# Kernel optimization log

Hardware: AMD Instinct MI355X
Metric: run time of the kernel (lower is better)

## Reference

```python
import jax, jax.numpy as jnp
import numpy as np

NSAMPLE = 32
EPS = 1e-5


def _fps(xyz, npoint):
    # xyz: [B, N, 3] -> indices [B, npoint] (farthest point sampling, start at idx 0)
    B, N, _ = xyz.shape
    def body(i, state):
        idx, dist, far = state
        idx = idx.at[:, i].set(far)
        centroid = jnp.take_along_axis(xyz, far[:, None, None], axis=1)  # [B,1,3]
        d = jnp.sum((xyz - centroid) ** 2, axis=-1)                      # [B,N]
        dist = jnp.minimum(dist, d)
        far = jnp.argmax(dist, axis=-1).astype(jnp.int32)
        return idx, dist, far
    idx0 = jnp.zeros((B, npoint), jnp.int32)
    dist0 = jnp.full((B, N), 1e10, xyz.dtype)
    far0 = jnp.zeros((B,), jnp.int32)
    idx, _, _ = jax.lax.fori_loop(0, npoint, body, (idx0, dist0, far0))
    return idx


def _knn(query, ref, k):
    # query [B,S,3], ref [B,N,3] -> neighbor idx [B,S,k]
    d = (jnp.sum(query * query, -1)[:, :, None]
         - 2.0 * jnp.einsum('bsc,bnc->bsn', query, ref)
         + jnp.sum(ref * ref, -1)[:, None, :])
    _, idx = jax.lax.top_k(-d, k)
    return idx


def _gather(x, idx):
    # x [B,N,C], idx [B,S,K] -> [B,S,K,C]
    B, S, K = idx.shape
    out = jnp.take_along_axis(x, idx.reshape(B, S * K)[..., None], axis=1)
    return out.reshape(B, S, K, x.shape[-1])


def _set_abstraction(xyz, feat, npoint, weights):
    # xyz [B,N,3], feat [B,N,C]
    fidx = _fps(xyz, npoint)
    new_xyz = jnp.take_along_axis(xyz, fidx[..., None], axis=1)        # [B,S,3]
    nidx = _knn(new_xyz, xyz, NSAMPLE)                                 # [B,S,K]
    g_xyz = _gather(xyz, nidx) - new_xyz[:, :, None, :]                # [B,S,K,3]
    g_feat = _gather(feat, nidx)                                       # [B,S,K,C]
    x = jnp.concatenate([g_xyz, g_feat], axis=-1)                      # [B,S,K,3+C]
    for W in weights:  # 1x1 conv == per-point matmul, then InstanceNorm2d (affine=False) + ReLU
        x = jnp.einsum('bskc,cd->bskd', x, W)
        mu = jnp.mean(x, axis=(1, 2), keepdims=True)
        var = jnp.var(x, axis=(1, 2), keepdims=True)
        x = jax.nn.relu((x - mu) * jax.lax.rsqrt(var + EPS))
    new_feat = jnp.max(x, axis=2)                                      # [B,S,Cout]
    return new_xyz, new_feat, fidx


def setup_inputs() -> dict:
    key = jax.random.key(0)
    ks = jax.random.split(key, 8)
    B, N = 4, 16384
    pc = jax.random.normal(ks[0], (B, 3, N), jnp.float32)
    feature = jax.random.normal(ks[1], (B, 3, N), jnp.float32)
    def w(k, cin, cout):
        return jax.random.normal(k, (cin, cout), jnp.float32) / np.sqrt(cin).astype(np.float32)
    return {
        'pc': pc, 'feature': feature,
        'sa1_w1': w(ks[2], 6, 32),  'sa1_w2': w(ks[3], 32, 32), 'sa1_w3': w(ks[4], 32, 32),
        'sa2_w1': w(ks[5], 35, 64), 'sa2_w2': w(ks[6], 64, 64), 'sa2_w3': w(ks[7], 64, 64),
    }


def reference(pc, feature, sa1_w1, sa1_w2, sa1_w3, sa2_w1, sa2_w2, sa2_w3):
    NPOINT = 4096
    xyz = jnp.transpose(pc, (0, 2, 1))       # [B,N,3]
    feat = jnp.transpose(feature, (0, 2, 1))  # [B,N,3]
    xyz1, feat1, fidx1 = _set_abstraction(xyz, feat, NPOINT // 2, [sa1_w1, sa1_w2, sa1_w3])
    xyz2, feat2, fidx2 = _set_abstraction(xyz1, feat1, NPOINT // 4, [sa2_w1, sa2_w2, sa2_w3])
    # match torch channel-first layout on outputs
    pc_l1 = jnp.transpose(xyz1, (0, 2, 1))
    pc_l2 = jnp.transpose(xyz2, (0, 2, 1))
    feat_l2 = jnp.transpose(feat2, (0, 2, 1))  # [B,64,NPOINT//4]
    return (pc, pc_l1, pc_l2, feat_l2, fidx1, fidx2)
```

## Files before the change

kernel.cpp:

```cpp
#include <hip/hip_runtime.h>
#include <math.h>

namespace {

constexpr int BB = 4;
constexpr int N0 = 16384;
constexpr int S1 = 2048;
constexpr int S2 = 1024;

__device__ __forceinline__ float sq3(float x, float y, float z){
  #pragma clang fp contract(off)
  return x*x + y*y + z*z;
}
__device__ __forceinline__ float sqdist(float ax,float ay,float az,float bx,float by,float bz){
  #pragma clang fp contract(off)
  float dx = ax-bx; float dy = ay-by; float dz = az-bz;
  return dx*dx + dy*dy + dz*dz;
}
__device__ __forceinline__ float dot3(float ax,float ay,float az,float bx,float by,float bz){
  #pragma clang fp contract(off)
  return ax*bx + ay*by + az*bz;
}
__device__ __forceinline__ float knndist(float qs, float dot, float rs){
  #pragma clang fp contract(off)
  return (qs - 2.0f*dot) + rs;
}

__global__ __launch_bounds__(256) void k_setup(const float* __restrict__ pc,
                                               const float* __restrict__ feat,
                                               float* __restrict__ out_pc,
                                               float* __restrict__ xyz,
                                               float* __restrict__ fN,
                                               float* __restrict__ rsq0)
{
  int t = blockIdx.x*256 + threadIdx.x;
  if (t < BB*3*N0) out_pc[t] = pc[t];
  if (t < BB*N0){
    int b = t >> 14, n = t & (N0-1);
    const float* p = pc + (size_t)b*3*N0;
    float x = p[n], y = p[N0+n], z = p[2*N0+n];
    float* q = xyz + (size_t)t*3;
    q[0]=x; q[1]=y; q[2]=z;
    rsq0[t] = sq3(x,y,z);
    const float* f = feat + (size_t)b*3*N0;
    float* g = fN + (size_t)t*3;
    g[0]=f[n]; g[1]=f[N0+n]; g[2]=f[2*N0+n];
  }
}

__device__ __forceinline__ void fps_writeout(int b, int i, float cx, float cy, float cz, int far,
                                             float* sxyz, float* srsq, float* pcl, float* fidxf, int NP)
{
  fidxf[(size_t)b*NP + i] = (float)far;
  float* o = sxyz + ((size_t)b*NP + i)*3;
  o[0]=cx; o[1]=cy; o[2]=cz;
  float* pb = pcl + (size_t)b*3*NP;
  pb[i] = cx; pb[NP+i] = cy; pb[2*NP+i] = cz;
  srsq[(size_t)b*NP + i] = sq3(cx,cy,cz);
}

template<int N, int NP, int BS, int PPT>
__global__ __launch_bounds__(BS, 2) void k_fps(const float* __restrict__ pts,
                                               float* __restrict__ sxyz,
                                               float* __restrict__ srsq,
                                               float* __restrict__ pcl,
                                               float* __restrict__ fidxf)
{
  static_assert(N == BS*PPT, "bad fps shape");
  constexpr int NW = BS/64;
  int b = blockIdx.x, t = threadIdx.x;
  int lane = t & 63;
  int wid  = t >> 6;
  const float* P = pts + (size_t)b*N*3;

  __shared__ unsigned long long slot[2][NW];

  float px[PPT], py[PPT], pz[PPT], dist[PPT];
  #pragma unroll
  for (int j=0;j<PPT;j++){
    int g = t + BS*j;
    px[j]=P[g*3]; py[j]=P[g*3+1]; pz[j]=P[g*3+2];
    asm volatile("" : "+v"(px[j]), "+v"(py[j]), "+v"(pz[j]));
    dist[j]=1e10f;
  }

  float cx = P[0], cy = P[1], cz = P[2];
  if (t == 0) fps_writeout(b, 0, cx, cy, cz, 0, sxyz, srsq, pcl, fidxf, NP);

  for (int i=1;i<NP;i++){
    int par = i & 1;
    float msq = -1.0f;
    #pragma unroll
    for (int j=0;j<PPT;j++){
      float d  = sqdist(px[j],py[j],pz[j],cx,cy,cz);
      float nd = fminf(dist[j], d);
      dist[j]  = nd;
      msq = fmaxf(msq, nd);
    }
    #pragma unroll
    for (int off=32; off>0; off>>=1) msq = fmaxf(msq, __shfl_xor(msq, off));
    float s = sqrtf(msq);
    unsigned xb = __float_as_uint(msq);
    while (xb > 0u && sqrtf(__uint_as_float(xb - 1u)) == s) xb--;
    float lo = __uint_as_float(xb);
    int li = 0x7FFFFFFF;
    #pragma unroll
    for (int j=PPT-1;j>=0;j--) if (dist[j] >= lo) li = t + BS*j;
    #pragma unroll
    for (int off=32; off>0; off>>=1) li = min(li, __shfl_xor(li, off));
    if (lane == 0)
      slot[par][wid] = ((unsigned long long)__float_as_uint(s) << 32)
                     | (unsigned long long)(unsigned)(~li);
    __syncthreads();
    unsigned long long best = slot[par][0];
    #pragma unroll
    for (int w=1; w<NW; w++){
      unsigned long long o = slot[par][w];
      best = (o > best) ? o : best;
    }
    int far = (int)(~(unsigned)best);
    far = __builtin_amdgcn_readfirstlane(far);
    cx = P[(size_t)far*3]; cy = P[(size_t)far*3+1]; cz = P[(size_t)far*3+2];
    if (t == 0) fps_writeout(b, i, cx, cy, cz, far, sxyz, srsq, pcl, fidxf, NP);
  }
}

template<int NREF, int PPT, int NQ>
__global__ __launch_bounds__(512) void k_knn(const float* __restrict__ qxyz,
                                             const float* __restrict__ qrsq,
                                             const float* __restrict__ rxyz,
                                             const float* __restrict__ rrsq,
                                             int* __restrict__ nidx)
{
  static_assert(NREF == 512*PPT, "bad knn shape");
  int q = blockIdx.x;
  int b = q / NQ;
  int t = threadIdx.x;
  const float* R  = rxyz + (size_t)b*NREF*3;
  const float* RS = rrsq + (size_t)b*NREF;
  float qx = qxyz[(size_t)q*3], qy = qxyz[(size_t)q*3+1], qz = qxyz[(size_t)q*3+2];
  float qs = qrsq[q];
  unsigned u[PPT];
  #pragma unroll
  for (int j=0;j<PPT;j++){
    int g = t + 512*j;
    float rx=R[g*3], ry=R[g*3+1], rz=R[g*3+2];
    float d = knndist(qs, dot3(qx,qy,qz,rx,ry,rz), RS[g]);
    unsigned bu = __float_as_uint(d);
    u[j] = ((int)bu < 0) ? ~bu : (bu | 0x80000000u);
  }
  __shared__ unsigned hist[256];
  __shared__ unsigned s_pref, s_pm, s_want, s_cnteq;
  __shared__ int s_n;
  __shared__ int s_eq[1024];
  __shared__ int s_ne;
  if (t == 0){ s_pref=0u; s_pm=0u; s_want=32u; s_n=0; s_ne=0; }

  for (int shift=24; shift>=0; shift-=8){
    if (t < 256) hist[t] = 0u;
    __syncthreads();
    unsigned pref = s_pref, pm = s_pm;
    #pragma unroll
    for (int j=0;j<PPT;j++){
      if ((u[j] & pm) == pref) atomicAdd(&hist[(u[j]>>shift)&255], 1u);
    }
    __syncthreads();
    if (t < 64){
      unsigned h0=hist[4*t], h1=hist[4*t+1], h2=hist[4*t+2], h3=hist[4*t+3];
      unsigned ssum = h0+h1+h2+h3;
      unsigned inc = ssum;
      #pragma unroll
      for (int off=1; off<64; off<<=1){
        unsigned o = __shfl_up(inc, off);
        if (t >= off) inc += o;
      }
      unsigned exc = inc - ssum;
      unsigned want = s_want;
      if (exc < want && want <= inc){
        unsigned rem = want - exc;
        unsigned bin, below;
        if      (rem <= h0)       { bin=4*t+0; below=exc; }
        else if (rem <= h0+h1)    { bin=4*t+1; below=exc+h0; }
        else if (rem <= h0+h1+h2) { bin=4*t+2; below=exc+h0+h1; }
        else                      { bin=4*t+3; below=exc+h0+h1+h2; }
        s_pref = pref | (bin << shift);
        s_pm   = pm   | (0xFFu << shift);
        s_want = want - below;
        if (shift == 0) s_cnteq = hist[bin];
      }
    }
    __syncthreads();
  }
  unsigned T = s_pref;
  unsigned krem = s_want;
  unsigned cnteq = s_cnteq;
  int* outq = nidx + (size_t)q*32;
  #pragma unroll
  for (int j=0;j<PPT;j++){
    if (u[j] < T){ int p = atomicAdd(&s_n, 1); outq[p] = t + 512*j; }
  }
  __syncthreads();
  if (cnteq == krem){
    #pragma unroll
    for (int j=0;j<PPT;j++){
      if (u[j] == T){ int p = atomicAdd(&s_n, 1); outq[p] = t + 512*j; }
    }
  } else {
    #pragma unroll
    for (int j=0;j<PPT;j++){
      if (u[j] == T){ int p = atomicAdd(&s_ne, 1); if (p < 1024) s_eq[p] = t + 512*j; }
    }
    __syncthreads();
    if (t == 0){
      int ne = s_ne; if (ne > 1024) ne = 1024;
      int p = s_n;
      int take = (int)krem; if (take > ne) take = ne;
      for (int r=0; r<take; r++){
        int mn = 0x7FFFFFFF, mi = -1;
        for (int e=0; e<ne; e++){ if (s_eq[e] < mn){ mn = s_eq[e]; mi = e; } }
        if (mi < 0) break;
        outq[p++] = mn;
        s_eq[mi] = 0x7FFFFFFF;
      }
    }
  }
}

template<int C>
__device__ __forceinline__ void accum_sums(const float* o, int b, float* sums){
  __shared__ float s_sum[C];
  __shared__ float s_ssq[C];
  int t = threadIdx.x;
  if (t < C){ s_sum[t]=0.f; s_ssq[t]=0.f; }
  __syncthreads();
  int lane = t & 63;
  #pragma unroll
  for (int c=0;c<C;c++){
    float v = o[c], v2 = v*v;
    #pragma unroll
    for (int off=32; off>0; off>>=1){ v += __shfl_down(v, off); v2 += __shfl_down(v2, off); }
    if (lane == 0){ atomicAdd(&s_sum[c], v); atomicAdd(&s_ssq[c], v2); }
  }
  __syncthreads();
  if (t < C){
    atomicAdd(&sums[(b*64+t)*2],   s_sum[t]);
    atomicAdd(&sums[(b*64+t)*2+1], s_ssq[t]);
  }
}

__global__ __launch_bounds__(256) void k_sa1_l1(const float* __restrict__ xyz,
                                                const float* __restrict__ fN,
                                                const float* __restrict__ sxyz,
                                                const int* __restrict__ nidx,
                                                const float* __restrict__ W,
                                                float* __restrict__ xout,
                                                float* __restrict__ sums)
{
  __shared__ float sW[192];
  int t = threadIdx.x;
  if (t < 192) sW[t] = W[t];
  int row = blockIdx.x*256 + t;
  int b = row >> 16;
  int sk = row & 65535;
  int s = sk >> 5;
  int nb = nidx[row];
  const float* pr = xyz  + ((size_t)(b*N0 + nb))*3;
  const float* pq = sxyz + ((size_t)(b*S1 + s ))*3;
  const float* pf = fN   + ((size_t)(b*N0 + nb))*3;
  float i0 = pr[0]-pq[0], i1 = pr[1]-pq[1], i2 = pr[2]-pq[2];
  float i3 = pf[0], i4 = pf[1], i5 = pf[2];
  __syncthreads();
  float o[32];
  #pragma unroll
  for (int c=0;c<32;c++){
    float a = i0*sW[c];
    a = fmaf(i1, sW[ 32+c], a);
    a = fmaf(i2, sW[ 64+c], a);
    a = fmaf(i3, sW[ 96+c], a);
    a = fmaf(i4, sW[128+c], a);
    a = fmaf(i5, sW[160+c], a);
    o[c] = a;
    xout[(size_t)c*262144 + row] = a;
  }
  accum_sums<32>(o, b, sums);
}

template<int CIN, int COUT, int LRPB>
__global__ __launch_bounds__(256) void k_sa_mid(const float* __restrict__ xin,
                                                const float* __restrict__ W,
                                                const float* __restrict__ sums_in,
                                                float* __restrict__ xout,
                                                float* __restrict__ sums_out,
                                                int rows_total, float invM)
{
  __shared__ float sW[CIN*COUT];
  __shared__ float s_mu[CIN];
  __shared__ float s_rs[CIN];
  int t = threadIdx.x;
  int row = blockIdx.x*256 + t;
  int bb = (blockIdx.x*256) >> LRPB;
  for (int i=t; i<CIN*COUT; i+=256) sW[i] = W[i];
  if (t < CIN){
    float sm = sums_in[(bb*64+t)*2], sq = sums_in[(bb*64+t)*2+1];
    float mu = sm*invM;
    float var = fmaxf(sq*invM - mu*mu, 0.f);
    s_mu[t] = mu;
    s_rs[t] = 1.0f/sqrtf(var + 1e-5f);
  }
  __syncthreads();
  float o[COUT];
  #pragma unroll
  for (int d=0;d<COUT;d++) o[d] = 0.f;
  #pragma unroll
  for (int c=0;c<CIN;c++){
    float x = xin[(size_t)c*rows_total + row];
    float v = fmaxf((x - s_mu[c])*s_rs[c], 0.f);
    #pragma unroll
    for (int d=0;d<COUT;d++) o[d] = fmaf(v, sW[c*COUT+d], o[d]);
  }
  #pragma unroll
  for (int d=0;d<COUT;d++) xout[(size_t)d*rows_total + row] = o[d];
  accum_sums<COUT>(o, bb, sums_out);
}

__global__ __launch_bounds__(256) void k_sa2_l1(const float* __restrict__ xyz1,
                                                const float* __restrict__ feat1,
                                                const float* __restrict__ xyz2,
                                                const int* __restrict__ nidx,
                                                const float* __restrict__ W,
                                                float* __restrict__ xout,
                                                float* __restrict__ sums)
{
  __shared__ float sW[35*64];
  int t = threadIdx.x;
  for (int i=t; i<35*64; i+=256) sW[i] = W[i];
  int row = blockIdx.x*256 + t;
  int b = row >> 15;
  int sk = row & 32767;
  int s = sk >> 5;
  int nb = nidx[row];
  const float* pr = xyz1 + ((size_t)(b*S1 + nb))*3;
  const float* pq = xyz2 + ((size_t)(b*S2 + s ))*3;
  const float* pf = feat1 + ((size_t)(b*S1 + nb))*32;
  float i0 = pr[0]-pq[0], i1 = pr[1]-pq[1], i2 = pr[2]-pq[2];
  float fv[32];
  #pragma unroll
  for (int c=0;c<32;c++) fv[c] = pf[c];
  __syncthreads();
  float o[64];
  #pragma unroll
  for (int d=0;d<64;d++){
    float a = i0*sW[d];
    a = fmaf(i1, sW[ 64+d], a);
    a = fmaf(i2, sW[128+d], a);
    o[d] = a;
  }
  #pragma unroll
  for (int c=0;c<32;c++){
    float v = fv[c];
    #pragma unroll
    for (int d=0;d<64;d++) o[d] = fmaf(v, sW[(3+c)*64+d], o[d]);
  }
  #pragma unroll
  for (int d=0;d<64;d++) xout[(size_t)d*131072 + row] = o[d];
  accum_sums<64>(o, b, sums);
}

template<int C, int PTSB, int CF>
__global__ __launch_bounds__(256) void k_pool(const float* __restrict__ xin,
                                              const float* __restrict__ sums_in,
                                              float* __restrict__ out,
                                              int rows_total, float invM)
{
  int t = threadIdx.x;
  int c = t & (C-1);
  int pl = t / C;
  int p = blockIdx.x*(256/C) + pl;
  int b = p / PTSB;
  float sm = sums_in[(b*64+c)*2], sq = sums_in[(b*64+c)*2+1];
  float mu = sm*invM;
  float var = fmaxf(sq*invM - mu*mu, 0.f);
  float rs = 1.0f/sqrtf(var + 1e-5f);
  const float* xp = xin + (size_t)c*rows_total + (size_t)p*32;
  float m = -1e30f;
  #pragma unroll
  for (int k=0;k<32;k++) m = fmaxf(m, xp[k]);
  m = fmaxf((m - mu)*rs, 0.0f);
  if (CF) out[((size_t)(b*C + c))*PTSB + (p - b*PTSB)] = m;
  else    out[(size_t)p*C + c] = m;
}

constexpr size_t WS_XYZ   = 0;
constexpr size_t WS_FN    = WS_XYZ   + 196608;
constexpr size_t WS_RSQ0  = WS_FN    + 196608;
constexpr size_t WS_XYZ1  = WS_RSQ0  + 65536;
constexpr size_t WS_RSQ1  = WS_XYZ1  + 24576;
constexpr size_t WS_XYZ2  = WS_RSQ1  + 8192;
constexpr size_t WS_RSQ2  = WS_XYZ2  + 12288;
constexpr size_t WS_FEAT1 = WS_RSQ2  + 4096;
constexpr size_t WS_SUMS  = WS_FEAT1 + 262144;
constexpr size_t WS_BUFA  = WS_SUMS  + 3072;
constexpr size_t WS_BUFB  = WS_BUFA  + 8388608;
constexpr size_t WS_NIDX1 = WS_BUFB  + 8388608;
constexpr size_t WS_NIDX2 = WS_NIDX1 + 262144;

constexpr size_t OUT1 = 196608;
constexpr size_t OUT2 = 221184;
constexpr size_t OUT3 = 233472;
constexpr size_t OUT4 = 495616;
constexpr size_t OUT5 = 503808;

}

extern "C" void kernel_launch(void* const* d_in, const int* in_sizes, int n_in,
                              void* d_out, int out_size, void* d_ws, size_t ws_size,
                              hipStream_t stream)
{
  (void)in_sizes; (void)n_in; (void)out_size; (void)ws_size;
  const float* pc   = (const float*)d_in[0];
  const float* feat = (const float*)d_in[1];
  const float* W1 = (const float*)d_in[2];
  const float* W2 = (const float*)d_in[3];
  const float* W3 = (const float*)d_in[4];
  const float* W4 = (const float*)d_in[5];
  const float* W5 = (const float*)d_in[6];
  const float* W6 = (const float*)d_in[7];
  float* out = (float*)d_out;
  float* ws  = (float*)d_ws;

  float* xyz   = ws + WS_XYZ;
  float* fN    = ws + WS_FN;
  float* rsq0  = ws + WS_RSQ0;
  float* xyz1  = ws + WS_XYZ1;
  float* rsq1  = ws + WS_RSQ1;
  float* xyz2  = ws + WS_XYZ2;
  float* rsq2  = ws + WS_RSQ2;
  float* feat1 = ws + WS_FEAT1;
  float* sums  = ws + WS_SUMS;
  float* bufA  = ws + WS_BUFA;
  float* bufB  = ws + WS_BUFB;
  int* nidx1   = (int*)(ws + WS_NIDX1);
  int* nidx2   = (int*)(ws + WS_NIDX2);

  (void)hipMemsetAsync(sums, 0, 3072*sizeof(float), stream);

  k_setup<<<768, 256, 0, stream>>>(pc, feat, out, xyz, fN, rsq0);

  k_fps<N0, S1, 512, 32><<<BB, 512, 0, stream>>>(xyz, xyz1, rsq1, out+OUT1, out+OUT4);
  k_knn<N0, 32, S1><<<BB*S1, 512, 0, stream>>>(xyz1, rsq1, xyz, rsq0, nidx1);
  k_sa1_l1<<<1024, 256, 0, stream>>>(xyz, fN, xyz1, nidx1, W1, bufA, sums);
  k_sa_mid<32,32,16><<<1024, 256, 0, stream>>>(bufA, W2, sums,       bufB, sums+512,  262144, 1.0f/65536.0f);
  k_sa_mid<32,32,16><<<1024, 256, 0, stream>>>(bufB, W3, sums+512,   bufA, sums+1024, 262144, 1.0f/65536.0f);
  k_pool<32, 2048, 0><<<1024, 256, 0, stream>>>(bufA, sums+1024, feat1, 262144, 1.0f/65536.0f);

  k_fps<S1, S2, 512, 4><<<BB, 512, 0, stream>>>(xyz1, xyz2, rsq2, out+OUT2, out+OUT5);
  k_knn<S1, 4, S2><<<BB*S2, 512, 0, stream>>>(xyz2, rsq2, xyz1, rsq1, nidx2);
  k_sa2_l1<<<512, 256, 0, stream>>>(xyz1, feat1, xyz2, nidx2, W4, bufB, sums+1536);
  k_sa_mid<64,64,15><<<512, 256, 0, stream>>>(bufB, W5, sums+1536, bufA, sums+2048, 131072, 1.0f/32768.0f);
  k_sa_mid<64,64,15><<<512, 256, 0, stream>>>(bufA, W6, sums+2048, bufB, sums+2560, 131072, 1.0f/32768.0f);
  k_pool<64, 1024, 1><<<1024, 256, 0, stream>>>(bufB, sums+2560, out+OUT3, 131072, 1.0f/32768.0f);
}
```

Measured before the change: 7.167 ms.

## Morton-sort points and skip FPS distance updates via per-thread bounding-box bounds

Before the first farthest-point sampling, points are binned into a 16^3 Morton grid and sorted by counting sort (histogram, scan, scatter). The new FPS kernel gives each thread 16 spatially coherent points and keeps their bounding box. A thread skips its distance update whenever the new centroid's lower-bound distance to that box cannot beat the thread's current max. Points are re-read from global memory each iteration and a permutation in shared memory maps sorted slots back to original indices. This adds three small kernels and extra memory traffic, and the quantisation assumes coordinates lie roughly in [-5,5]; values outside are clamped, which only affects how tight the pruning is.

```diff
diff --git a/kernel.cpp b/kernel.cpp
--- a/kernel.cpp
+++ b/kernel.cpp
@@ -59,34 +59,185 @@
   srsq[(size_t)b*NP + i] = sq3(cx,cy,cz);
 }
 
-template<int N, int NP, int BS, int PPT>
-__global__ __launch_bounds__(BS, 2) void k_fps(const float* __restrict__ pts,
+__device__ __forceinline__ int fps_quant(float v){
+  int q = (int)((v + 5.0f) * 1.6f);
+  return q < 0 ? 0 : (q > 15 ? 15 : q);
+}
+__device__ __forceinline__ int fps_mort(int qx,int qy,int qz){
+  int c = 0;
+  #pragma unroll
+  for (int i=0;i<4;i++){
+    c |= (((qx>>i)&1)<<(3*i)) | (((qy>>i)&1)<<(3*i+1)) | (((qz>>i)&1)<<(3*i+2));
+  }
+  return c;
+}
+
+__global__ __launch_bounds__(256) void k_cell(const float* __restrict__ xyz,
+                                              int* __restrict__ cellid,
+                                              unsigned* __restrict__ hist)
+{
+  int t = blockIdx.x*256 + threadIdx.x;
+  int b = t >> 14;
+  const float* p = xyz + (size_t)t*3;
+  int code = fps_mort(fps_quant(p[0]), fps_quant(p[1]), fps_quant(p[2]));
+  cellid[t] = code;
+  atomicAdd(&hist[b*4096 + code], 1u);
+}
+
+__global__ __launch_bounds__(1024) void k_scan(const unsigned* __restrict__ hist,
+                                               unsigned* __restrict__ cstart)
+{
+  int b = blockIdx.x, t = threadIdx.x, lane = t & 63, wid = t >> 6;
+  unsigned v0 = hist[b*4096 + 4*t+0];
+  unsigned v1 = hist[b*4096 + 4*t+1];
+  unsigned v2 = hist[b*4096 + 4*t+2];
+  unsigned v3 = hist[b*4096 + 4*t+3];
+  unsigned s = v0+v1+v2+v3;
+  unsigned inc = s;
+  #pragma unroll
+  for (int off=1; off<64; off<<=1){
+    unsigned o = __shfl_up(inc, off);
+    if (lane >= off) inc += o;
+  }
+  __shared__ unsigned wsum[16];
+  if (lane == 63) wsum[wid] = inc;
+  __syncthreads();
+  unsigned woff = 0;
+  #pragma unroll
+  for (int w=0; w<16; w++) if (w < wid) woff += wsum[w];
+  unsigned exc = woff + (inc - s);
+  cstart[b*4096 + 4*t+0] = exc;
+  cstart[b*4096 + 4*t+1] = exc + v0;
+  cstart[b*4096 + 4*t+2] = exc + v0 + v1;
+  cstart[b*4096 + 4*t+3] = exc + v0 + v1 + v2;
+}
+
+__global__ __launch_bounds__(256) void k_scatter(const float* __restrict__ xyz,
+                                                 const int* __restrict__ cellid,
+                                                 const unsigned* __restrict__ cstart,
+                                                 unsigned* __restrict__ ccur,
+                                                 float* __restrict__ srtxyz,
+                                                 int* __restrict__ perm)
+{
+  int t = blockIdx.x*256 + threadIdx.x;
+  int b = t >> 14, n = t & (N0-1);
+  int code = cellid[t];
+  unsigned pos = cstart[b*4096 + code] + atomicAdd(&ccur[b*4096 + code], 1u);
+  size_t d = (size_t)b*N0 + pos;
+  const float* p = xyz + (size_t)t*3;
+  float* o = srtxyz + d*3;
+  o[0]=p[0]; o[1]=p[1]; o[2]=p[2];
+  perm[d] = n;
+}
+
+__global__ __launch_bounds__(1024) void k_fps1(const float* __restrict__ srtxyz,
+                                               const int* __restrict__ permg,
+                                               const float* __restrict__ xyz,
                                                float* __restrict__ sxyz,
                                                float* __restrict__ srsq,
                                                float* __restrict__ pcl,
                                                float* __restrict__ fidxf)
 {
+  constexpr int NP = S1;
+  constexpr int NW = 16;
+  int b = blockIdx.x, t = threadIdx.x;
+  int lane = t & 63, wid = t >> 6;
+  const float* S  = srtxyz + (size_t)b*N0*3;
+  const int*   PM = permg  + (size_t)b*N0;
+  const float* PO = xyz    + (size_t)b*N0*3;
+
+  __shared__ int s_perm[N0];
+  __shared__ unsigned long long slot[2][NW];
+  for (int i=t; i<N0; i+=1024) s_perm[i] = PM[i];
+
+  float dist[16];
+  float bxmin=1e30f,bxmax=-1e30f,bymin=1e30f,bymax=-1e30f,bzmin=1e30f,bzmax=-1e30f;
+  #pragma unroll
+  for (int j=0;j<16;j++){
+    const float* pp = S + (size_t)(t*16+j)*3;
+    float x=pp[0], y=pp[1], z=pp[2];
+    bxmin=fminf(bxmin,x); bxmax=fmaxf(bxmax,x);
+    bymin=fminf(bymin,y); bymax=fmaxf(bymax,y);
+    bzmin=fminf(bzmin,z); bzmax=fmaxf(bzmax,z);
+    dist[j] = 1e10f;
+  }
+  float bmax = 1e10f;
+  __syncthreads();
+
+  float cx = PO[0], cy = PO[1], cz = PO[2];
+  if (t == 0) fps_writeout(b, 0, cx, cy, cz, 0, sxyz, srsq, pcl, fidxf, NP);
+
+  for (int i=1;i<NP;i++){
+    int par = i & 1;
+    float qx = fminf(fmaxf(cx, bxmin), bxmax);
+    float qy = fminf(fmaxf(cy, bymin), bymax);
+    float qz = fminf(fmaxf(cz, bzmin), bzmax);
+    float lb = sqdist(qx,qy,qz,cx,cy,cz);
+    if (lb*0.99999f < bmax){
+      float nm = -1.0f;
+      #pragma unroll
+      for (int j=0;j<16;j++){
+        const float* pp = S + (size_t)(t*16+j)*3;
+        float d  = sqdist(pp[0],pp[1],pp[2],cx,cy,cz);
+        float nd = fminf(dist[j], d);
+        dist[j]  = nd;
+        nm = fmaxf(nm, nd);
+      }
+      bmax = nm;
+    }
+    float msq = bmax;
+    #pragma unroll
+    for (int off=32; off>0; off>>=1) msq = fmaxf(msq, __shfl_xor(msq, off));
+    float s = sqrtf(msq);
+    unsigned xb = __float_as_uint(msq);
+    while (xb > 0u && sqrtf(__uint_as_float(xb - 1u)) == s) xb--;
+    float lo = __uint_as_float(xb);
+    int li = 0x7FFFFFFF;
+    if (bmax >= lo){
+      #pragma unroll
+      for (int j=0;j<16;j++) if (dist[j] >= lo) li = min(li, s_perm[t*16+j]);
+    }
+    #pragma unroll
+    for (int off=32; off>0; off>>=1) li = min(li, __shfl_xor(li, off));
+    if (lane == 0)
+      slot[par][wid] = ((unsigned long long)__float_as_uint(s) << 32)
+                     | (unsigned long long)(unsigned)(~li);
+    __syncthreads();
+    unsigned long long best = slot[par][0];
+    #pragma unroll
+    for (int w=1; w<NW; w++){
+      unsigned long long o = slot[par][w];
+      best = (o > best) ? o : best;
+    }
+    int far = (int)(~(unsigned)best);
+    far = __builtin_amdgcn_readfirstlane(far);
+    cx = PO[(size_t)far*3]; cy = PO[(size_t)far*3+1]; cz = PO[(size_t)far*3+2];
+    if (t == 0) fps_writeout(b, i, cx, cy, cz, far, sxyz, srsq, pcl, fidxf, NP);
+  }
+}
+
+template<int N, int NP, int BS, int PPT>
+__global__ __launch_bounds__(BS) void k_fps_scan(const float* __restrict__ pts,
+                                                 float* __restrict__ sxyz,
+                                                 float* __restrict__ srsq,
+                                                 float* __restrict__ pcl,
+                                                 float* __restrict__ fidxf)
+{
   static_assert(N == BS*PPT, "bad fps shape");
   constexpr int NW = BS/64;
   int b = blockIdx.x, t = threadIdx.x;
-  int lane = t & 63;
-  int wid  = t >> 6;
+  int lane = t & 63, wid = t >> 6;
   const float* P = pts + (size_t)b*N*3;
-
   __shared__ unsigned long long slot[2][NW];
-
   float px[PPT], py[PPT], pz[PPT], dist[PPT];
   #pragma unroll
   for (int j=0;j<PPT;j++){
     int g = t + BS*j;
     px[j]=P[g*3]; py[j]=P[g*3+1]; pz[j]=P[g*3+2];
-    asm volatile("" : "+v"(px[j]), "+v"(py[j]), "+v"(pz[j]));
     dist[j]=1e10f;
   }
-
   float cx = P[0], cy = P[1], cz = P[2];
   if (t == 0) fps_writeout(b, 0, cx, cy, cz, 0, sxyz, srsq, pcl, fidxf, NP);
-
   for (int i=1;i<NP;i++){
     int par = i & 1;
     float msq = -1.0f;
@@ -404,6 +555,13 @@
 constexpr size_t WS_NIDX1 = WS_BUFB  + 8388608;
 constexpr size_t WS_NIDX2 = WS_NIDX1 + 262144;
 
+constexpr size_t SRT_XYZ    = 0;
+constexpr size_t SRT_PERM   = 196608;
+constexpr size_t SRT_CELL   = 262144;
+constexpr size_t SRT_HIST   = 327680;
+constexpr size_t SRT_CSTART = 344064;
+constexpr size_t SRT_CCUR   = 360448;
+
 constexpr size_t OUT1 = 196608;
 constexpr size_t OUT2 = 221184;
 constexpr size_t OUT3 = 233472;
@@ -442,18 +600,29 @@
   int* nidx1   = (int*)(ws + WS_NIDX1);
   int* nidx2   = (int*)(ws + WS_NIDX2);
 
+  float*    srtxyz = bufA + SRT_XYZ;
+  int*      perm   = (int*)     (bufA + SRT_PERM);
+  int*      cellid = (int*)     (bufA + SRT_CELL);
+  unsigned* hist   = (unsigned*)(bufA + SRT_HIST);
+  unsigned* cstart = (unsigned*)(bufA + SRT_CSTART);
+  unsigned* ccur   = (unsigned*)(bufA + SRT_CCUR);
+
   (void)hipMemsetAsync(sums, 0, 3072*sizeof(float), stream);
+  (void)hipMemsetAsync(bufA + SRT_HIST, 0, 3*16384*sizeof(unsigned), stream);
 
   k_setup<<<768, 256, 0, stream>>>(pc, feat, out, xyz, fN, rsq0);
 
-  k_fps<N0, S1, 512, 32><<<BB, 512, 0, stream>>>(xyz, xyz1, rsq1, out+OUT1, out+OUT4);
+  k_cell   <<<256, 256, 0, stream>>>(xyz, cellid, hist);
+  k_scan   <<<BB, 1024, 0, stream>>>(hist, cstart);
+  k_scatter<<<256, 256, 0, stream>>>(xyz, cellid, cstart, ccur, srtxyz, perm);
+  k_fps1   <<<BB, 1024, 0, stream>>>(srtxyz, perm, xyz, xyz1, rsq1, out+OUT1, out+OUT4);
   k_knn<N0, 32, S1><<<BB*S1, 512, 0, stream>>>(xyz1, rsq1, xyz, rsq0, nidx1);
   k_sa1_l1<<<1024, 256, 0, stream>>>(xyz, fN, xyz1, nidx1, W1, bufA, sums);
   k_sa_mid<32,32,16><<<1024, 256, 0, stream>>>(bufA, W2, sums,       bufB, sums+512,  262144, 1.0f/65536.0f);
   k_sa_mid<32,32,16><<<1024, 256, 0, stream>>>(bufB, W3, sums+512,   bufA, sums+1024, 262144, 1.0f/65536.0f);
   k_pool<32, 2048, 0><<<1024, 256, 0, stream>>>(bufA, sums+1024, feat1, 262144, 1.0f/65536.0f);
 
-  k_fps<S1, S2, 512, 4><<<BB, 512, 0, stream>>>(xyz1, xyz2, rsq2, out+OUT2, out+OUT5);
+  k_fps_scan<S1, S2, 512, 4><<<BB, 512, 0, stream>>>(xyz1, xyz2, rsq2, out+OUT2, out+OUT5);
   k_knn<S1, 4, S2><<<BB*S2, 512, 0, stream>>>(xyz2, rsq2, xyz1, rsq1, nidx2);
   k_sa2_l1<<<512, 256, 0, stream>>>(xyz1, feat1, xyz2, nidx2, W4, bufB, sums+1536);
   k_sa_mid<64,64,15><<<512, 256, 0, stream>>>(bufB, W5, sums+1536, bufA, sums+2048, 131072, 1.0f/32768.0f);
```

Result: slower. 8.379 ms (+16.9%).
